# Performance work log

Measured on AMD Instinct MI355X. Metric: run time of the kernel, lower is better.

Reference implementation:

```python
import jax, jax.numpy as jnp
import numpy as np

BS, N, L, H, E, W, K = 32, 512, 4096, 256, 64, 8, 9
NE = 2048            # edges per graph
CIN = H + 2 * E + W  # pc1 input channels
CS = K // 2          # center slice start
LC = L - (K - 1)     # valid-conv output length
EPS = 1e-5


def setup_inputs() -> dict:
    key = jax.random.key(0)
    ks = jax.random.split(key, 12)
    s = 0.05
    d = {}
    d["x"] = jax.random.normal(ks[0], (BS, N, H), jnp.float32)
    d["edge_feat"] = jax.random.normal(ks[1], (BS, NE, E), jnp.float32)
    d["walk_nodes"] = jax.random.randint(ks[2], (BS, L), 0, N - 1)
    d["walk_edges"] = jax.random.randint(ks[3], (BS, L - 1), 0, NE)
    d["encodings"] = jax.random.normal(ks[4], (BS, W, L), jnp.float32)
    d["ln_g"] = jnp.ones((H,), jnp.float32)
    d["ln_b"] = jnp.zeros((H,), jnp.float32)
    d["pc1_w"] = jax.random.normal(ks[5], (2 * H, CIN), jnp.float32) * s
    d["pc1_b"] = jnp.zeros((2 * H,), jnp.float32)
    d["dc_w"] = jax.random.normal(ks[6], (H, K), jnp.float32) * s
    d["bn_g"] = jnp.ones((H,), jnp.float32)
    d["bn_b"] = jnp.zeros((H,), jnp.float32)
    d["pc2_w"] = jax.random.normal(ks[7], (H, H), jnp.float32) * s
    d["pc2_b"] = jnp.zeros((H,), jnp.float32)
    d["mlp_w1"] = jax.random.normal(ks[8], (H, H), jnp.float32) * s
    d["bn2_g"] = jnp.ones((H,), jnp.float32)
    d["bn2_b"] = jnp.zeros((H,), jnp.float32)
    d["mlp_w2"] = jax.random.normal(ks[9], (H, H), jnp.float32) * s
    return d


def reference(x, edge_feat, walk_nodes, walk_edges, encodings,
              ln_g, ln_b, pc1_w, pc1_b, dc_w, bn_g, bn_b,
              pc2_w, pc2_b, mlp_w1, bn2_g, bn2_b, mlp_w2):
    # LayerNorm over hidden dim
    mu = x.mean(-1, keepdims=True)
    var = x.var(-1, keepdims=True)
    xn = (x - mu) * jax.lax.rsqrt(var + EPS) * ln_g + ln_b

    vn = xn[:, 0]  # [BS, H]

    # gather walk node features: x[batch, walk_nodes+1] -> [BS, H, L]
    xg = jnp.take_along_axis(xn, (walk_nodes + 1)[:, :, None], axis=1)
    xg = xg.transpose(0, 2, 1)

    # gather walk edge features -> [BS, E, L-1], pad to in/out channels of len L
    we = jnp.take_along_axis(edge_feat, walk_edges[:, :, None], axis=1).transpose(0, 2, 1)
    pad = jnp.zeros((BS, E, 1), xg.dtype)
    we_i = jnp.concatenate([pad, we], axis=2)
    we_o = jnp.concatenate([we, pad], axis=2)

    h = jnp.concatenate([xg, we_i, we_o, encodings], axis=1)  # [BS, CIN, L]

    # pointwise conv 1 + GLU
    h = jnp.einsum('oc,bcl->bol', pc1_w, h) + pc1_b[None, :, None]
    out, gate = jnp.split(h, 2, axis=1)
    h = out * jax.nn.sigmoid(gate)  # [BS, H, L]

    # depthwise conv, VALID -> [BS, H, LC]
    h = jax.lax.conv_general_dilated(
        h, dc_w[:, None, :], window_strides=(1,), padding='VALID',
        feature_group_count=H, dimension_numbers=('NCH', 'OIH', 'NCH'))

    # BatchNorm1d (training mode, biased var over batch+length)
    m = h.mean((0, 2))
    v = h.var((0, 2))
    h = (h - m[None, :, None]) * jax.lax.rsqrt(v + EPS)[None, :, None] \
        * bn_g[None, :, None] + bn_b[None, :, None]

    # Swish + pointwise conv 2
    h = h * jax.nn.sigmoid(h)
    h = jnp.einsum('oc,bcl->bol', pc2_w, h) + pc2_b[None, :, None]
    h = h.transpose(0, 2, 1)  # [BS, LC, H]

    # scatter_mean over center nodes into n-1 real-node slots
    center = jax.lax.dynamic_slice_in_dim(walk_nodes, CS, LC, axis=1)  # [BS, LC]
    flat_idx = (center + jnp.arange(BS, dtype=center.dtype)[:, None] * (N - 1)).reshape(-1)
    sums = jax.ops.segment_sum(h.reshape(BS * LC, H), flat_idx, num_segments=BS * (N - 1))
    cnt = jax.ops.segment_sum(jnp.ones((BS * LC,), h.dtype), flat_idx, num_segments=BS * (N - 1))
    node_out = (sums / jnp.maximum(cnt, 1.0)[:, None]).reshape(BS, N - 1, H)

    # virtual node MLP: Linear -> BN -> ReLU -> Linear
    z = (vn + node_out.sum(1)) @ mlp_w1.T
    m2 = z.mean(0)
    v2 = z.var(0)
    z = (z - m2) * jax.lax.rsqrt(v2 + EPS) * bn2_g + bn2_b
    z = jax.nn.relu(z) @ mlp_w2.T
    vn_out = z[:, None]  # [BS, 1, H]

    return jnp.concatenate([vn_out, node_out + vn_out], axis=1)  # [BS, N, H]
```

## Files before the change

### kernel.cpp

```cpp
#include <hip/hip_runtime.h>
#include <hip/hip_bf16.h>

typedef __hip_bfloat16 bf16;
typedef __attribute__((ext_vector_type(8))) short short8v;
typedef __attribute__((ext_vector_type(4))) float f32x4;

#define BS 32
#define NN 512
#define LL 4096
#define HH 256
#define EE 64
#define WW 8
#define KK 9
#define NE 2048
#define CIN 392
#define KP 416
#define FS 424
#define FS2 264
#define LC 4088
#define NM1 511
#define CR 128
#define K2M 64
#define K5M 64

__device__ __forceinline__ float b2f(bf16 v) { return __bfloat162float(v); }
__device__ __forceinline__ float bfr(unsigned short u) {
    union { unsigned int i; float f; } cv; cv.i = ((unsigned int)u) << 16; return cv.f;
}
__device__ __forceinline__ unsigned short f2b(float v) {
    return __builtin_bit_cast(unsigned short, __float2bfloat16(v));
}
__device__ __forceinline__ unsigned int pack2(float a, float b) {
    return (unsigned int)f2b(a) | ((unsigned int)f2b(b) << 16);
}
__device__ __forceinline__ float sigm(float x) {
    return __builtin_amdgcn_rcpf(1.f + __expf(-x));
}

__global__ void k0_all(const float* __restrict__ pc1w, const float* __restrict__ pc2w,
                       const float* __restrict__ edge, unsigned short* __restrict__ wb,
                       unsigned short* __restrict__ w2b, unsigned short* __restrict__ eb) {
    size_t i = (size_t)blockIdx.x * 256 + threadIdx.x;
    eb[i] = f2b(edge[i]);
    if (i < (size_t)512 * KP) {
        int row = (int)(i / KP), c = (int)(i % KP);
        wb[i] = (c < CIN) ? f2b(pc1w[(size_t)row * CIN + c]) : 0;
    }
    if (i < (size_t)HH * HH) w2b[i] = f2b(pc2w[i]);
}

__global__ void k1_layernorm(const float* __restrict__ x, const float* __restrict__ ln_g,
                             const float* __restrict__ ln_b, unsigned short* __restrict__ xnb,
                             float* __restrict__ acc) {
    int b = blockIdx.y, n = blockIdx.x, t = threadIdx.x;
    size_t base = ((size_t)(b * NN + n)) * HH;
    float v = x[base + t];
    __shared__ float s1[4], s2[4], mv[2];
    float a = v, q = v * v;
    #pragma unroll
    for (int o = 32; o > 0; o >>= 1) { a += __shfl_down(a, o, 64); q += __shfl_down(q, o, 64); }
    if ((t & 63) == 0) { s1[t >> 6] = a; s2[t >> 6] = q; }
    __syncthreads();
    if (t == 0) {
        float sa = s1[0] + s1[1] + s1[2] + s1[3];
        float sq = s2[0] + s2[1] + s2[2] + s2[3];
        float mean = sa * (1.0f / 256.0f);
        float var = sq * (1.0f / 256.0f) - mean * mean;
        mv[0] = mean; mv[1] = rsqrtf(var + 1e-5f);
    }
    __syncthreads();
    float outv = (v - mv[0]) * mv[1] * ln_g[t] + ln_b[t];
    xnb[base + t] = f2b(outv);
    if (n == 0) acc[b * HH + t] = outv;
}

__global__ void kb_all(const int* __restrict__ wn, int* __restrict__ offs,
                       int* __restrict__ bins) {
    __shared__ int cnt[NM1];
    __shared__ int cur[NM1];
    __shared__ int ps[256];
    int b = blockIdx.x, t = threadIdx.x;
    for (int i = t; i < NM1; i += 256) cnt[i] = 0;
    __syncthreads();
    for (int l = t; l < LC; l += 256)
        atomicAdd(&cnt[wn[b * LL + l + (KK / 2)]], 1);
    __syncthreads();
    int c0 = (2 * t < NM1)     ? cnt[2 * t]     : 0;
    int c1 = (2 * t + 1 < NM1) ? cnt[2 * t + 1] : 0;
    int pair = c0 + c1;
    ps[t] = pair;
    __syncthreads();
    for (int o = 1; o < 256; o <<= 1) {
        int add = (t >= o) ? ps[t - o] : 0;
        __syncthreads();
        ps[t] += add;
        __syncthreads();
    }
    int ex = ps[t] - pair;
    offs[b * 512 + 2 * t] = ex;
    offs[b * 512 + 2 * t + 1] = ex + c0;
    if (2 * t < NM1)     cur[2 * t]     = ex;
    if (2 * t + 1 < NM1) cur[2 * t + 1] = ex + c0;
    __syncthreads();
    for (int l = t; l < LC; l += 256) {
        int c = wn[b * LL + l + (KK / 2)];
        int slot = atomicAdd(&cur[c], 1);
        bins[b * LC + slot] = l;
    }
}

__global__ void __launch_bounds__(256, 2)
k2_mfma(const unsigned short* __restrict__ xnb, const unsigned short* __restrict__ edgeb,
        const int* __restrict__ wn, const int* __restrict__ we,
        const float* __restrict__ enc, const unsigned short* __restrict__ wb,
        const float* __restrict__ pc1_b, unsigned short* __restrict__ h1) {
    __shared__ __align__(16) unsigned short smem[K2M * FS];
    __shared__ int rown[K2M], ein[K2M], eout[K2M];
    int b = blockIdx.y, l0 = blockIdx.x * K2M, t = threadIdx.x;
    int lane = t & 63, wv = t >> 6;
    int l15 = lane & 15, lr = (lane >> 4) & 3, koff = lr * 8;
    int c0 = wv * 64;
    const unsigned short* wrO = wb + ((size_t)(c0 + l15)) * KP + koff;
    const unsigned short* wrG = wb + ((size_t)(HH + c0 + l15)) * KP + koff;

    short8v bo0[4], bg0[4], bo1[4], bg1[4];
    #pragma unroll
    for (int n = 0; n < 4; ++n) {
        bo0[n] = *(const short8v*)(wrO + (size_t)n * 16 * KP);
        bg0[n] = *(const short8v*)(wrG + (size_t)n * 16 * KP);
    }

    if (t < K2M) {
        int l = l0 + t;
        rown[t] = wn[b * LL + l] + 1;
        ein[t]  = (l > 0)      ? we[b * (LL - 1) + l - 1] : -1;
        eout[t] = (l < LL - 1) ? we[b * (LL - 1) + l]     : -1;
    }
    __syncthreads();

    for (int i = t; i < K2M * 32; i += 256) {
        int r = i >> 5, c = (i & 31) * 8;
        *(uint4*)&smem[r * FS + c] =
            *(const uint4*)(xnb + ((size_t)(b * NN + rown[r])) * HH + c);
    }
    for (int i = t; i < K2M * 16; i += 256) {
        int r = i >> 4, q = i & 15;
        int idx = (q < 8) ? ein[r] : eout[r];
        uint4 v = {0u, 0u, 0u, 0u};
        if (idx >= 0)
            v = *(const uint4*)(edgeb + ((size_t)(b * NE + idx)) * EE + (q & 7) * 8);
        *(uint4*)&smem[r * FS + HH + q * 8] = v;
    }
    for (int i = t; i < K2M * 5; i += 256) {
        int r = i / 5, q = i % 5;
        uint4 v = {0u, 0u, 0u, 0u};
        if (q == 0) {
            const float* ep = enc + (size_t)b * WW * LL + (l0 + r);
            v.x = pack2(ep[0], ep[LL]);          v.y = pack2(ep[2 * LL], ep[3 * LL]);
            v.z = pack2(ep[4 * LL], ep[5 * LL]); v.w = pack2(ep[6 * LL], ep[7 * LL]);
        }
        *(uint4*)&smem[r * FS + (HH + 2 * EE) + q * 8] = v;
    }
    __syncthreads();

    f32x4 acc[4][8];
    #pragma unroll
    for (int m = 0; m < 4; ++m)
        #pragma unroll
        for (int n = 0; n < 8; ++n) acc[m][n] = (f32x4){0.f, 0.f, 0.f, 0.f};

    const unsigned short* arow = &smem[l15 * FS + koff];

    #pragma unroll 1
    for (int p = 0; p < 6; ++p) {
        int kk = 2 * p;
        #pragma unroll
        for (int n = 0; n < 4; ++n) {
            bo1[n] = *(const short8v*)(wrO + (size_t)n * 16 * KP + (kk + 1) * 32);
            bg1[n] = *(const short8v*)(wrG + (size_t)n * 16 * KP + (kk + 1) * 32);
        }
        {
            short8v a[4];
            #pragma unroll
            for (int m = 0; m < 4; ++m)
                a[m] = *(const short8v*)(arow + (size_t)m * 16 * FS + kk * 32);
            #pragma unroll
            for (int m = 0; m < 4; ++m)
                #pragma unroll
                for (int n = 0; n < 4; ++n) {
                    acc[m][n]     = __builtin_amdgcn_mfma_f32_16x16x32_bf16(a[m], bo0[n], acc[m][n], 0, 0, 0);
                    acc[m][n + 4] = __builtin_amdgcn_mfma_f32_16x16x32_bf16(a[m], bg0[n], acc[m][n + 4], 0, 0, 0);
                }
        }
        #pragma unroll
        for (int n = 0; n < 4; ++n) {
            bo0[n] = *(const short8v*)(wrO + (size_t)n * 16 * KP + (kk + 2) * 32);
            bg0[n] = *(const short8v*)(wrG + (size_t)n * 16 * KP + (kk + 2) * 32);
        }
        {
            short8v a[4];
            #pragma unroll
            for (int m = 0; m < 4; ++m)
                a[m] = *(const short8v*)(arow + (size_t)m * 16 * FS + (kk + 1) * 32);
            #pragma unroll
            for (int m = 0; m < 4; ++m)
                #pragma unroll
                for (int n = 0; n < 4; ++n) {
                    acc[m][n]     = __builtin_amdgcn_mfma_f32_16x16x32_bf16(a[m], bo1[n], acc[m][n], 0, 0, 0);
                    acc[m][n + 4] = __builtin_amdgcn_mfma_f32_16x16x32_bf16(a[m], bg1[n], acc[m][n + 4], 0, 0, 0);
                }
        }
    }
    {
        short8v a[4];
        #pragma unroll
        for (int m = 0; m < 4; ++m)
            a[m] = *(const short8v*)(arow + (size_t)m * 16 * FS + 12 * 32);
        #pragma unroll
        for (int m = 0; m < 4; ++m)
            #pragma unroll
            for (int n = 0; n < 4; ++n) {
                acc[m][n]     = __builtin_amdgcn_mfma_f32_16x16x32_bf16(a[m], bo0[n], acc[m][n], 0, 0, 0);
                acc[m][n + 4] = __builtin_amdgcn_mfma_f32_16x16x32_bf16(a[m], bg0[n], acc[m][n + 4], 0, 0, 0);
            }
    }

    float biasO[4], biasG[4];
    #pragma unroll
    for (int n = 0; n < 4; ++n) {
        biasO[n] = pc1_b[c0 + n * 16 + l15];
        biasG[n] = pc1_b[HH + c0 + n * 16 + l15];
    }

    __syncthreads();
    unsigned short* glu = smem;
    int cb = c0 + l15;
    #pragma unroll
    for (int m = 0; m < 4; ++m)
        #pragma unroll
        for (int n = 0; n < 4; ++n)
            #pragma unroll
            for (int r = 0; r < 4; ++r) {
                int pos = m * 16 + lr * 4 + r;
                float o = acc[m][n][r] + biasO[n];
                float g = acc[m][n + 4][r] + biasG[n];
                glu[pos * FS2 + cb + n * 16] = f2b(o * sigm(g));
            }
    __syncthreads();
    for (int i = t; i < K2M * 32; i += 256) {
        int r = i >> 5, c = (i & 31) * 8;
        *(uint4*)(h1 + ((size_t)(b * LL) + l0 + r) * HH + c) = *(const uint4*)&glu[r * FS2 + c];
    }
}

__global__ void k3f_conv_stats(const unsigned short* __restrict__ h1, const float* __restrict__ dc_w,
                               unsigned short* __restrict__ h2, float* __restrict__ bnsum,
                               float* __restrict__ bnsumsq) {
    __shared__ float sr[4][HH], qr[4][HH];
    int b = blockIdx.y, l0 = blockIdx.x * CR, t = threadIdx.x;
    int g = t >> 6, c4 = (t & 63) * 4;
    int rows_all = min(CR, LC - l0);
    int r0 = g * (CR / 4);
    int r1 = min(r0 + CR / 4, rows_all);

    float wk[4][KK];
    #pragma unroll
    for (int j = 0; j < 4; ++j)
        #pragma unroll
        for (int k = 0; k < KK; ++k) wk[j][k] = dc_w[(c4 + j) * KK + k];

    float s[4] = {0.f, 0.f, 0.f, 0.f}, q[4] = {0.f, 0.f, 0.f, 0.f};
    if (r0 < r1) {
        const unsigned short* src = h1 + ((size_t)b * LL + l0 + r0) * HH + c4;
        float w[KK][4];
        float nxt[4];
        #pragma unroll
        for (int k = 0; k < KK - 1; ++k) {
            uint2 v = *(const uint2*)(src + (size_t)k * HH);
            w[k][0] = bfr((unsigned short)(v.x & 0xffffu)); w[k][1] = bfr((unsigned short)(v.x >> 16));
            w[k][2] = bfr((unsigned short)(v.y & 0xffffu)); w[k][3] = bfr((unsigned short)(v.y >> 16));
        }
        {
            uint2 v = *(const uint2*)(src + (size_t)(KK - 1) * HH);
            nxt[0] = bfr((unsigned short)(v.x & 0xffffu)); nxt[1] = bfr((unsigned short)(v.x >> 16));
            nxt[2] = bfr((unsigned short)(v.y & 0xffffu)); nxt[3] = bfr((unsigned short)(v.y >> 16));
        }
        for (int i = r0; i < r1; ++i) {
            #pragma unroll
            for (int j = 0; j < 4; ++j) w[KK - 1][j] = nxt[j];
            if (i + 1 < r1) {
                uint2 v = *(const uint2*)(src + (size_t)(i - r0 + KK) * HH);
                nxt[0] = bfr((unsigned short)(v.x & 0xffffu)); nxt[1] = bfr((unsigned short)(v.x >> 16));
                nxt[2] = bfr((unsigned short)(v.y & 0xffffu)); nxt[3] = bfr((unsigned short)(v.y >> 16));
            }
            float o[4];
            #pragma unroll
            for (int j = 0; j < 4; ++j) {
                float v = 0.f;
                #pragma unroll
                for (int k = 0; k < KK; ++k) v += w[k][j] * wk[j][k];
                o[j] = v;
                s[j] += v; q[j] += v * v;
            }
            uint2 ov;
            ov.x = pack2(o[0], o[1]); ov.y = pack2(o[2], o[3]);
            *(uint2*)(h2 + ((size_t)b * LC + l0 + i) * HH + c4) = ov;
            #pragma unroll
            for (int k = 0; k < KK - 1; ++k)
                #pragma unroll
                for (int j = 0; j < 4; ++j) w[k][j] = w[k + 1][j];
        }
    }
    #pragma unroll
    for (int j = 0; j < 4; ++j) { sr[g][c4 + j] = s[j]; qr[g][c4 + j] = q[j]; }
    __syncthreads();
    float ss = sr[0][t] + sr[1][t] + sr[2][t] + sr[3][t];
    float qq = qr[0][t] + qr[1][t] + qr[2][t] + qr[3][t];
    atomicAdd(&bnsum[t], ss);
    atomicAdd(&bnsumsq[t], qq);
}

__global__ void k4b_finalize(const float* __restrict__ bnsum, const float* __restrict__ bnsumsq,
                             const float* __restrict__ bn_g, const float* __restrict__ bn_b,
                             float* __restrict__ bnscale, float* __restrict__ bnshift) {
    int c = threadIdx.x;
    const float M = (float)(BS * LC);
    float mean = bnsum[c] / M;
    float var = bnsumsq[c] / M - mean * mean;
    float rstd = rsqrtf(var + 1e-5f);
    float sc = rstd * bn_g[c];
    bnscale[c] = sc;
    bnshift[c] = bn_b[c] - mean * sc;
}

__global__ void __launch_bounds__(256, 3)
k5_mfma(const unsigned short* __restrict__ h2, const float* __restrict__ bnscale,
        const float* __restrict__ bnshift, const unsigned short* __restrict__ w2b,
        const float* __restrict__ pc2_b, unsigned short* __restrict__ h3) {
    __shared__ __align__(16) unsigned short smem[K5M * FS2];
    __shared__ float scl[HH], shl[HH];
    int b = blockIdx.y, l0 = blockIdx.x * K5M, t = threadIdx.x;
    int lane = t & 63, wv = t >> 6;
    int l15 = lane & 15, lr = (lane >> 4) & 3, koff = lr * 8;
    int c0 = wv * 64;
    const unsigned short* wrow = w2b + ((size_t)(c0 + l15)) * HH + koff;

    short8v b0[4], b1[4];
    #pragma unroll
    for (int n = 0; n < 4; ++n) b0[n] = *(const short8v*)(wrow + (size_t)n * 16 * HH);

    scl[t] = bnscale[t];
    shl[t] = bnshift[t];
    __syncthreads();

    for (int i = t; i < K5M * 32; i += 256) {
        int r = i >> 5, c = (i & 31) * 8;
        int l = l0 + r;
        uint4 out = {0u, 0u, 0u, 0u};
        if (l < LC) {
            uint4 v = *(const uint4*)(h2 + ((size_t)b * LC + l) * HH + c);
            unsigned int vv[4] = {v.x, v.y, v.z, v.w};
            unsigned int oo[4];
            #pragma unroll
            for (int j = 0; j < 4; ++j) {
                float f0 = bfr((unsigned short)(vv[j] & 0xffffu));
                float f1 = bfr((unsigned short)(vv[j] >> 16));
                float a0 = f0 * scl[c + 2 * j]     + shl[c + 2 * j];
                float a1 = f1 * scl[c + 2 * j + 1] + shl[c + 2 * j + 1];
                a0 = a0 * sigm(a0);
                a1 = a1 * sigm(a1);
                oo[j] = pack2(a0, a1);
            }
            out.x = oo[0]; out.y = oo[1]; out.z = oo[2]; out.w = oo[3];
        }
        *(uint4*)&smem[r * FS2 + c] = out;
    }
    __syncthreads();

    f32x4 acc[4][4];
    #pragma unroll
    for (int m = 0; m < 4; ++m)
        #pragma unroll
        for (int n = 0; n < 4; ++n) acc[m][n] = (f32x4){0.f, 0.f, 0.f, 0.f};

    const unsigned short* arow = &smem[l15 * FS2 + koff];

    #pragma unroll 1
    for (int p = 0; p < 4; ++p) {
        int kk = 2 * p;
        #pragma unroll
        for (int n = 0; n < 4; ++n)
            b1[n] = *(const short8v*)(wrow + (size_t)n * 16 * HH + (kk + 1) * 32);
        {
            short8v a[4];
            #pragma unroll
            for (int m = 0; m < 4; ++m)
                a[m] = *(const short8v*)(arow + (size_t)m * 16 * FS2 + kk * 32);
            #pragma unroll
            for (int m = 0; m < 4; ++m)
                #pragma unroll
                for (int n = 0; n < 4; ++n)
                    acc[m][n] = __builtin_amdgcn_mfma_f32_16x16x32_bf16(a[m], b0[n], acc[m][n], 0, 0, 0);
        }
        if (p < 3) {
            #pragma unroll
            for (int n = 0; n < 4; ++n)
                b0[n] = *(const short8v*)(wrow + (size_t)n * 16 * HH + (kk + 2) * 32);
        }
        {
            short8v a[4];
            #pragma unroll
            for (int m = 0; m < 4; ++m)
                a[m] = *(const short8v*)(arow + (size_t)m * 16 * FS2 + (kk + 1) * 32);
            #pragma unroll
            for (int m = 0; m < 4; ++m)
                #pragma unroll
                for (int n = 0; n < 4; ++n)
                    acc[m][n] = __builtin_amdgcn_mfma_f32_16x16x32_bf16(a[m], b1[n], acc[m][n], 0, 0, 0);
        }
    }

    int chb = c0 + l15;
    float bias[4];
    #pragma unroll
    for (int n = 0; n < 4; ++n) bias[n] = pc2_b[chb + n * 16];

    __syncthreads();
    #pragma unroll
    for (int m = 0; m < 4; ++m)
        #pragma unroll
        for (int n = 0; n < 4; ++n)
            #pragma unroll
            for (int r = 0; r < 4; ++r) {
                int pos = m * 16 + lr * 4 + r;
                smem[pos * FS2 + chb + n * 16] = f2b(acc[m][n][r] + bias[n]);
            }
    __syncthreads();
    for (int i = t; i < K5M * 32; i += 256) {
        int r = i >> 5, c = (i & 31) * 8;
        int l = l0 + r;
        if (l < LC)
            *(uint4*)(h3 + ((size_t)b * LC + l) * HH + c) = *(const uint4*)&smem[r * FS2 + c];
    }
}

__global__ void k6_gather(const unsigned short* __restrict__ h3, const int* __restrict__ offs,
                          const int* __restrict__ bins, float* __restrict__ node_out) {
    int bn = blockIdx.x;
    int b = bn / NM1, n = bn % NM1, t = threadIdx.x;
    int s = offs[b * 512 + n], e = offs[b * 512 + n + 1];
    float sum = 0.f;
    for (int i = s; i < e; ++i) {
        int l = bins[b * LC + i];
        sum += bfr(h3[((size_t)b * LC + l) * HH + t]);
    }
    float inv = 1.f / (float)max(e - s, 1);
    node_out[(size_t)bn * HH + t] = sum * inv;
}

__global__ void k6b_accsum(const float* __restrict__ node_out, float* __restrict__ acc) {
    int b = blockIdx.y, g = blockIdx.x, t = threadIdx.x;
    int n0 = g * 32, n1 = min(n0 + 32, NM1);
    float s = 0.f;
    for (int n = n0; n < n1; ++n) s += node_out[((size_t)b * NM1 + n) * HH + t];
    atomicAdd(&acc[b * HH + t], s);
}

__global__ void k7_mlp1(const float* __restrict__ acc, const float* __restrict__ w1,
                        float* __restrict__ z) {
    int b = blockIdx.x, t = threadIdx.x;
    __shared__ float a[HH];
    a[t] = acc[b * HH + t];
    __syncthreads();
    const float* w = w1 + (size_t)t * HH;
    float s = 0.f;
    for (int c = 0; c < HH; ++c) s += w[c] * a[c];
    z[b * HH + t] = s;
}

__global__ void k8_bn2(float* __restrict__ z, const float* __restrict__ g2,
                       const float* __restrict__ b2v) {
    int t = threadIdx.x;
    float vals[BS];
    float m = 0.f, q = 0.f;
    for (int b = 0; b < BS; ++b) {
        float v = z[b * HH + t];
        vals[b] = v; m += v; q += v * v;
    }
    m *= (1.0f / BS);
    q = q * (1.0f / BS) - m * m;
    float rstd = rsqrtf(q + 1e-5f);
    float sc = rstd * g2[t];
    float sh = b2v[t] - m * sc;
    for (int b = 0; b < BS; ++b) z[b * HH + t] = fmaxf(vals[b] * sc + sh, 0.f);
}

__global__ void k9_mlp2(const float* __restrict__ z, const float* __restrict__ w2,
                        float* __restrict__ vnout) {
    int b = blockIdx.x, t = threadIdx.x;
    __shared__ float a[HH];
    a[t] = z[b * HH + t];
    __syncthreads();
    const float* w = w2 + (size_t)t * HH;
    float s = 0.f;
    for (int c = 0; c < HH; ++c) s += w[c] * a[c];
    vnout[b * HH + t] = s;
}

__global__ void k10_out(const float* __restrict__ vnout, const float* __restrict__ node_out,
                        float* __restrict__ out) {
    int bn = blockIdx.x;
    int b = bn >> 9, n = bn & (NN - 1), t = threadIdx.x;
    float vo = vnout[b * HH + t];
    float v = (n == 0) ? vo : node_out[((size_t)b * NM1 + (n - 1)) * HH + t] + vo;
    out[(size_t)bn * HH + t] = v;
}

extern "C" void kernel_launch(void* const* d_in, const int* in_sizes, int n_in,
                              void* d_out, int out_size, void* d_ws, size_t ws_size,
                              hipStream_t stream) {
    const float* x     = (const float*)d_in[0];
    const float* edge  = (const float*)d_in[1];
    const int*   wn    = (const int*)d_in[2];
    const int*   we    = (const int*)d_in[3];
    const float* enc   = (const float*)d_in[4];
    const float* ln_g  = (const float*)d_in[5];
    const float* ln_b  = (const float*)d_in[6];
    const float* pc1_w = (const float*)d_in[7];
    const float* pc1_b = (const float*)d_in[8];
    const float* dc_w  = (const float*)d_in[9];
    const float* bn_g  = (const float*)d_in[10];
    const float* bn_b  = (const float*)d_in[11];
    const float* pc2_w = (const float*)d_in[12];
    const float* pc2_b = (const float*)d_in[13];
    const float* w1    = (const float*)d_in[14];
    const float* g2    = (const float*)d_in[15];
    const float* b2v   = (const float*)d_in[16];
    const float* w2    = (const float*)d_in[17];

    char* ws = (char*)d_ws;
    unsigned short* xnb   = (unsigned short*)(ws + 0);
    unsigned short* wbf   = (unsigned short*)(ws + 8388608);
    unsigned short* h1    = (unsigned short*)(ws + 8814592);
    unsigned short* h3    = h1;
    unsigned short* h2    = (unsigned short*)(ws + 75923456);
    float* node_out = (float*)(ws + 142901248);
    unsigned short* edgeb = (unsigned short*)(ws + 142901248);
    float* bnsum   = (float*)(ws + 159711104);
    float* bnsumsq = (float*)(ws + 159712128);
    float* acc     = (float*)(ws + 159713152);
    float* bnscale = (float*)(ws + 159745920);
    float* bnshift = (float*)(ws + 159746944);
    float* z       = (float*)(ws + 159747968);
    float* vnout   = (float*)(ws + 159780736);
    unsigned short* w2b = (unsigned short*)(ws + 159813504);
    int*   offs    = (int*)(ws + 159944576);
    int*   bins    = (int*)(ws + 160075520);

    hipMemsetAsync(ws + 159711104, 0, 2048, stream);

    k0_all<<<(BS * NE * EE) / 256, 256, 0, stream>>>(pc1_w, pc2_w, edge, wbf, w2b, edgeb);
    k1_layernorm<<<dim3(NN, BS), 256, 0, stream>>>(x, ln_g, ln_b, xnb, acc);
    kb_all<<<BS, 256, 0, stream>>>(wn, offs, bins);
    k2_mfma<<<dim3(LL / K2M, BS), 256, 0, stream>>>(xnb, edgeb, wn, we, enc, wbf, pc1_b, h1);
    k3f_conv_stats<<<dim3((LC + CR - 1) / CR, BS), 256, 0, stream>>>(h1, dc_w, h2, bnsum, bnsumsq);
    k4b_finalize<<<1, 256, 0, stream>>>(bnsum, bnsumsq, bn_g, bn_b, bnscale, bnshift);
    k5_mfma<<<dim3((LC + K5M - 1) / K5M, BS), 256, 0, stream>>>(h2, bnscale, bnshift, w2b, pc2_b, h3);
    k6_gather<<<BS * NM1, 256, 0, stream>>>(h3, offs, bins, node_out);
    k6b_accsum<<<dim3(16, BS), 256, 0, stream>>>(node_out, acc);
    k7_mlp1<<<BS, 256, 0, stream>>>(acc, w1, z);
    k8_bn2<<<1, 256, 0, stream>>>(z, g2, b2v);
    k9_mlp2<<<BS, 256, 0, stream>>>(z, w2, vnout);
    k10_out<<<BS * NN, 256, 0, stream>>>(vnout, node_out, (float*)d_out);
}
```

Before: 290.7 us.

## Remap blocks by XCD and fold small finalize kernels into consumers

Grids for the pc1 GEMM, depthwise conv and pc2 GEMM become one-dimensional, and block IDs are remapped so each XCD handles a contiguous set of batches. The goal is better L2 locality on the multi-die chip. BN finalize is folded into the pc2 kernel, BN2 is folded into the second MLP kernel, and the per-graph node sum moves into the gather kernel as atomics. Together these remove three launches. In exchange the BN stats are recomputed per block, and the gather now issues one atomic per node and channel, which adds contention.

```diff
diff --git a/kernel.cpp b/kernel.cpp
--- a/kernel.cpp
+++ b/kernel.cpp
@@ -116,7 +116,11 @@
         const float* __restrict__ pc1_b, unsigned short* __restrict__ h1) {
     __shared__ __align__(16) unsigned short smem[K2M * FS];
     __shared__ int rown[K2M], ein[K2M], eout[K2M];
-    int b = blockIdx.y, l0 = blockIdx.x * K2M, t = threadIdx.x;
+    int id = blockIdx.x;
+    int xcd = id & 7, s = id >> 3;
+    int b = xcd * 4 + (s >> 6);
+    int l0 = (s & 63) * K2M;
+    int t = threadIdx.x;
     int lane = t & 63, wv = t >> 6;
     int l15 = lane & 15, lr = (lane >> 4) & 3, koff = lr * 8;
     int c0 = wv * 64;
@@ -257,7 +261,11 @@
                                unsigned short* __restrict__ h2, float* __restrict__ bnsum,
                                float* __restrict__ bnsumsq) {
     __shared__ float sr[4][HH], qr[4][HH];
-    int b = blockIdx.y, l0 = blockIdx.x * CR, t = threadIdx.x;
+    int id = blockIdx.x;
+    int xcd = id & 7, s5 = id >> 3;
+    int b = xcd * 4 + (s5 >> 5);
+    int l0 = (s5 & 31) * CR;
+    int t = threadIdx.x;
     int g = t >> 6, c4 = (t & 63) * 4;
     int rows_all = min(CR, LC - l0);
     int r0 = g * (CR / 4);
@@ -320,26 +328,18 @@
     atomicAdd(&bnsumsq[t], qq);
 }
 
-__global__ void k4b_finalize(const float* __restrict__ bnsum, const float* __restrict__ bnsumsq,
-                             const float* __restrict__ bn_g, const float* __restrict__ bn_b,
-                             float* __restrict__ bnscale, float* __restrict__ bnshift) {
-    int c = threadIdx.x;
-    const float M = (float)(BS * LC);
-    float mean = bnsum[c] / M;
-    float var = bnsumsq[c] / M - mean * mean;
-    float rstd = rsqrtf(var + 1e-5f);
-    float sc = rstd * bn_g[c];
-    bnscale[c] = sc;
-    bnshift[c] = bn_b[c] - mean * sc;
-}
-
 __global__ void __launch_bounds__(256, 3)
-k5_mfma(const unsigned short* __restrict__ h2, const float* __restrict__ bnscale,
-        const float* __restrict__ bnshift, const unsigned short* __restrict__ w2b,
+k5_mfma(const unsigned short* __restrict__ h2, const float* __restrict__ bnsum,
+        const float* __restrict__ bnsumsq, const float* __restrict__ bn_g,
+        const float* __restrict__ bn_b, const unsigned short* __restrict__ w2b,
         const float* __restrict__ pc2_b, unsigned short* __restrict__ h3) {
     __shared__ __align__(16) unsigned short smem[K5M * FS2];
     __shared__ float scl[HH], shl[HH];
-    int b = blockIdx.y, l0 = blockIdx.x * K5M, t = threadIdx.x;
+    int id = blockIdx.x;
+    int xcd = id & 7, s = id >> 3;
+    int b = xcd * 4 + (s >> 6);
+    int l0 = (s & 63) * K5M;
+    int t = threadIdx.x;
     int lane = t & 63, wv = t >> 6;
     int l15 = lane & 15, lr = (lane >> 4) & 3, koff = lr * 8;
     int c0 = wv * 64;
@@ -349,8 +349,15 @@
     #pragma unroll
     for (int n = 0; n < 4; ++n) b0[n] = *(const short8v*)(wrow + (size_t)n * 16 * HH);
 
-    scl[t] = bnscale[t];
-    shl[t] = bnshift[t];
+    {
+        const float M = (float)(BS * LC);
+        float mean = bnsum[t] / M;
+        float var = bnsumsq[t] / M - mean * mean;
+        float rstd = rsqrtf(var + 1e-5f);
+        float sc = rstd * bn_g[t];
+        scl[t] = sc;
+        shl[t] = bn_b[t] - mean * sc;
+    }
     __syncthreads();
 
     for (int i = t; i < K5M * 32; i += 256) {
@@ -445,7 +452,8 @@
 }
 
 __global__ void k6_gather(const unsigned short* __restrict__ h3, const int* __restrict__ offs,
-                          const int* __restrict__ bins, float* __restrict__ node_out) {
+                          const int* __restrict__ bins, float* __restrict__ node_out,
+                          float* __restrict__ acc) {
     int bn = blockIdx.x;
     int b = bn / NM1, n = bn % NM1, t = threadIdx.x;
     int s = offs[b * 512 + n], e = offs[b * 512 + n + 1];
@@ -455,15 +463,9 @@
         sum += bfr(h3[((size_t)b * LC + l) * HH + t]);
     }
     float inv = 1.f / (float)max(e - s, 1);
-    node_out[(size_t)bn * HH + t] = sum * inv;
-}
-
-__global__ void k6b_accsum(const float* __restrict__ node_out, float* __restrict__ acc) {
-    int b = blockIdx.y, g = blockIdx.x, t = threadIdx.x;
-    int n0 = g * 32, n1 = min(n0 + 32, NM1);
-    float s = 0.f;
-    for (int n = n0; n < n1; ++n) s += node_out[((size_t)b * NM1 + n) * HH + t];
-    atomicAdd(&acc[b * HH + t], s);
+    float v = sum * inv;
+    node_out[(size_t)bn * HH + t] = v;
+    atomicAdd(&acc[b * HH + t], v);
 }
 
 __global__ void k7_mlp1(const float* __restrict__ acc, const float* __restrict__ w1,
@@ -478,28 +480,22 @@
     z[b * HH + t] = s;
 }
 
-__global__ void k8_bn2(float* __restrict__ z, const float* __restrict__ g2,
-                       const float* __restrict__ b2v) {
-    int t = threadIdx.x;
-    float vals[BS];
+__global__ void k9_mlp2(const float* __restrict__ z, const float* __restrict__ g2,
+                        const float* __restrict__ b2v, const float* __restrict__ w2,
+                        float* __restrict__ vnout) {
+    int b = blockIdx.x, t = threadIdx.x;
+    __shared__ float a[HH];
     float m = 0.f, q = 0.f;
-    for (int b = 0; b < BS; ++b) {
-        float v = z[b * HH + t];
-        vals[b] = v; m += v; q += v * v;
+    for (int bb = 0; bb < BS; ++bb) {
+        float v = z[bb * HH + t];
+        m += v; q += v * v;
     }
     m *= (1.0f / BS);
     q = q * (1.0f / BS) - m * m;
     float rstd = rsqrtf(q + 1e-5f);
     float sc = rstd * g2[t];
     float sh = b2v[t] - m * sc;
-    for (int b = 0; b < BS; ++b) z[b * HH + t] = fmaxf(vals[b] * sc + sh, 0.f);
-}
-
-__global__ void k9_mlp2(const float* __restrict__ z, const float* __restrict__ w2,
-                        float* __restrict__ vnout) {
-    int b = blockIdx.x, t = threadIdx.x;
-    __shared__ float a[HH];
-    a[t] = z[b * HH + t];
+    a[t] = fmaxf(z[b * HH + t] * sc + sh, 0.f);
     __syncthreads();
     const float* w = w2 + (size_t)t * HH;
     float s = 0.f;
@@ -549,8 +545,6 @@
     float* bnsum   = (float*)(ws + 159711104);
     float* bnsumsq = (float*)(ws + 159712128);
     float* acc     = (float*)(ws + 159713152);
-    float* bnscale = (float*)(ws + 159745920);
-    float* bnshift = (float*)(ws + 159746944);
     float* z       = (float*)(ws + 159747968);
     float* vnout   = (float*)(ws + 159780736);
     unsigned short* w2b = (unsigned short*)(ws + 159813504);
@@ -562,14 +556,11 @@
     k0_all<<<(BS * NE * EE) / 256, 256, 0, stream>>>(pc1_w, pc2_w, edge, wbf, w2b, edgeb);
     k1_layernorm<<<dim3(NN, BS), 256, 0, stream>>>(x, ln_g, ln_b, xnb, acc);
     kb_all<<<BS, 256, 0, stream>>>(wn, offs, bins);
-    k2_mfma<<<dim3(LL / K2M, BS), 256, 0, stream>>>(xnb, edgeb, wn, we, enc, wbf, pc1_b, h1);
-    k3f_conv_stats<<<dim3((LC + CR - 1) / CR, BS), 256, 0, stream>>>(h1, dc_w, h2, bnsum, bnsumsq);
-    k4b_finalize<<<1, 256, 0, stream>>>(bnsum, bnsumsq, bn_g, bn_b, bnscale, bnshift);
-    k5_mfma<<<dim3((LC + K5M - 1) / K5M, BS), 256, 0, stream>>>(h2, bnscale, bnshift, w2b, pc2_b, h3);
-    k6_gather<<<BS * NM1, 256, 0, stream>>>(h3, offs, bins, node_out);
-    k6b_accsum<<<dim3(16, BS), 256, 0, stream>>>(node_out, acc);
+    k2_mfma<<<(LL / K2M) * BS, 256, 0, stream>>>(xnb, edgeb, wn, we, enc, wbf, pc1_b, h1);
+    k3f_conv_stats<<<32 * BS, 256, 0, stream>>>(h1, dc_w, h2, bnsum, bnsumsq);
+    k5_mfma<<<(LL / K5M) * BS, 256, 0, stream>>>(h2, bnsum, bnsumsq, bn_g, bn_b, w2b, pc2_b, h3);
+    k6_gather<<<BS * NM1, 256, 0, stream>>>(h3, offs, bins, node_out, acc);
     k7_mlp1<<<BS, 256, 0, stream>>>(acc, w1, z);
-    k8_bn2<<<1, 256, 0, stream>>>(z, g2, b2v);
-    k9_mlp2<<<BS, 256, 0, stream>>>(z, w2, vnout);
+    k9_mlp2<<<BS, 256, 0, stream>>>(z, g2, b2v, w2, vnout);
     k10_out<<<BS * NN, 256, 0, stream>>>(vnout, node_out, (float*)d_out);
 }
```

Result: slower. 315.8 us (+8.6%).
